# Kernel tuning notes

Measured on AMD Instinct MI355X. Metric: run time of the kernel, lower is better.

## Reference

```python
import jax, jax.numpy as jnp
import numpy as np

KH, KW = 3, 3  # kernel_size


def _extract_patches(x, kh, kw):
    # x: (B, Ci, H, W) -> patches: (B, Ci, kh*kw, H, W)
    # Matches torch.nn.functional.unfold channel-major, kernel row-major order.
    B, Ci, H, W = x.shape
    ph, pw = kh // 2, kw // 2
    xp = jnp.pad(x, ((0, 0), (0, 0), (ph, ph), (pw, pw)))
    shifts = [xp[:, :, i:i + H, j:j + W] for i in range(kh) for j in range(kw)]
    return jnp.stack(shifts, axis=2)  # (B, Ci, K, H, W)


def setup_inputs() -> dict:
    key = jax.random.key(0)
    k1, k2 = jax.random.split(key)
    B, Ci, Co, H, W = 2, 32, 32, 64, 64
    K = KH * KW
    input = jax.random.normal(k1, (B, Ci, H, W), dtype=jnp.float32)
    weights = jax.random.normal(k2, (B, Ci, K, Co, H, W), dtype=jnp.float32)
    return {"input": input, "weights": weights}


def reference(input, weights):
    # input:   (B, Ci, H, W)
    # weights: (B, Ci, K, Co, H, W) with K = KH*KW
    patches = _extract_patches(input, KH, KW)            # (B, Ci, K, H, W)
    # Per-pixel GEMV: out[b,o,h,w] = sum_{c,k} patches[b,c,k,h,w] * weights[b,c,k,o,h,w]
    out = jnp.einsum('bckhw,bckohw->bohw', patches, weights)
    return out
```

## Files before the change

kernel.cpp:

```cpp
#include <hip/hip_runtime.h>

constexpr int B  = 2;
constexpr int Ci = 32;
constexpr int K  = 9;
constexpr int Co = 32;
constexpr int H  = 64;
constexpr int W  = 64;

typedef float f32x4 __attribute__((ext_vector_type(4)));

__global__ __launch_bounds__(256) void glc2d_kernel(
    const float* __restrict__ input,
    const float* __restrict__ weights,
    float* __restrict__ out)
{
    __shared__ f32x4 partial[3][64];

    const int tid = threadIdx.x;
    const int q   = tid & 63;
    const int cq  = tid >> 6;
    const int g   = blockIdx.x * 64 + q;

    const int w4 = g & 15;
    const int h  = (g >> 4) & (H - 1);
    const int o  = (g >> 10) & (Co - 1);
    const int b  = g >> 15;
    const int w0 = w4 * 4;

    float acc0 = 0.f, acc1 = 0.f, acc2 = 0.f, acc3 = 0.f;

    const size_t plane = (size_t)H * W;
    const size_t cstride = (size_t)K * Co * plane;
    const size_t kstride = (size_t)Co * plane;

    const int c0 = cq * 8;
    const float* wp = weights + ((size_t)(b * Ci + c0) * K) * Co * plane
                              + (size_t)o * plane + (size_t)h * W + w0;
    const float* ip = input + ((size_t)b * Ci + c0) * plane + (size_t)h * W + w0;

    const bool has_left  = (w4 > 0);
    const bool has_right = (w4 < 15);

#pragma unroll 2
    for (int c = 0; c < 8; ++c) {
        const float* wcp = wp + (size_t)c * cstride;
        f32x4 wv[9];
#pragma unroll
        for (int k = 0; k < 9; ++k) {
            wv[k] = __builtin_nontemporal_load(
                reinterpret_cast<const f32x4*>(wcp + (size_t)k * kstride));
        }

        const float* icp = ip + (size_t)c * plane;
        float row[3][6];
#pragma unroll
        for (int r = 0; r < 3; ++r) {
            const int hh = h + r - 1;
            const bool hok = (hh >= 0) & (hh < H);
            f32x4 v;
            if (hok) {
                v = *reinterpret_cast<const f32x4*>(icp + (size_t)(r - 1) * W);
            } else {
                v = (f32x4)(0.f);
            }
            const float lf = __shfl_up(v.w, 1);
            const float rt = __shfl_down(v.x, 1);
            row[r][0] = has_left  ? lf : 0.f;
            row[r][1] = v.x;
            row[r][2] = v.y;
            row[r][3] = v.z;
            row[r][4] = v.w;
            row[r][5] = has_right ? rt : 0.f;
        }

#pragma unroll
        for (int k = 0; k < 9; ++k) {
            const int r = k / 3;
            const int qq = k % 3;
            acc0 = fmaf(row[r][qq + 0], wv[k].x, acc0);
            acc1 = fmaf(row[r][qq + 1], wv[k].y, acc1);
            acc2 = fmaf(row[r][qq + 2], wv[k].z, acc2);
            acc3 = fmaf(row[r][qq + 3], wv[k].w, acc3);
        }
    }

    f32x4 acc;
    acc.x = acc0; acc.y = acc1; acc.z = acc2; acc.w = acc3;
    if (cq) {
        partial[cq - 1][q] = acc;
    }
    __syncthreads();
    if (!cq) {
        const f32x4 p0 = partial[0][q];
        const f32x4 p1 = partial[1][q];
        const f32x4 p2 = partial[2][q];
        acc += p0 + p1 + p2;
        const size_t oidx = ((((size_t)b * Co + o) * H + h) * W + w0);
        *reinterpret_cast<f32x4*>(out + oidx) = acc;
    }
}

extern "C" void kernel_launch(void* const* d_in, const int* in_sizes, int n_in,
                              void* d_out, int out_size, void* d_ws, size_t ws_size,
                              hipStream_t stream)
{
    const float* input   = (const float*)d_in[0];
    const float* weights = (const float*)d_in[1];
    float* out = (float*)d_out;

    const int total_threads = B * Co * H * (W / 4) * 4;
    const int block = 256;
    const int grid = total_threads / block;
    glc2d_kernel<<<grid, block, 0, stream>>>(input, weights, out);
}
```

Before: 50.68 us.

## Split channel reduction across eight thread groups and stream weights per kernel row

The Ci reduction is now split 8 ways instead of 4: each 256-thread block handles 32 output slots, with eight groups of 4 channels each, and the grid doubles. Weight loads are issued per kernel row (3 vectors) rather than all 9 up front, which lowers register pressure, and launch bounds now request 8 blocks per CU. The aim is more waves in flight to hide memory latency on this bandwidth-bound weight stream. The cost is wider 32-lane shuffles within a wave, a larger final LDS reduction and fewer loads in flight per thread.

```diff
diff --git a/kernel.cpp b/kernel.cpp
--- a/kernel.cpp
+++ b/kernel.cpp
@@ -9,17 +9,17 @@
 
 typedef float f32x4 __attribute__((ext_vector_type(4)));
 
-__global__ __launch_bounds__(256) void glc2d_kernel(
+__global__ __launch_bounds__(256, 8) void glc2d_kernel(
     const float* __restrict__ input,
     const float* __restrict__ weights,
     float* __restrict__ out)
 {
-    __shared__ f32x4 partial[3][64];
+    __shared__ f32x4 partial[7][32];
 
-    const int tid = threadIdx.x;
-    const int q   = tid & 63;
-    const int cq  = tid >> 6;
-    const int g   = blockIdx.x * 64 + q;
+    const int tid  = threadIdx.x;
+    const int slot = tid & 31;
+    const int cq   = tid >> 5;
+    const int g    = blockIdx.x * 32 + slot;
 
     const int w4 = g & 15;
     const int h  = (g >> 4) & (H - 1);
@@ -33,7 +33,7 @@
     const size_t cstride = (size_t)K * Co * plane;
     const size_t kstride = (size_t)Co * plane;
 
-    const int c0 = cq * 8;
+    const int c0 = cq * 4;
     const float* wp = weights + ((size_t)(b * Ci + c0) * K) * Co * plane
                               + (size_t)o * plane + (size_t)h * W + w0;
     const float* ip = input + ((size_t)b * Ci + c0) * plane + (size_t)h * W + w0;
@@ -41,20 +41,19 @@
     const bool has_left  = (w4 > 0);
     const bool has_right = (w4 < 15);
 
-#pragma unroll 2
-    for (int c = 0; c < 8; ++c) {
+    for (int c = 0; c < 4; ++c) {
         const float* wcp = wp + (size_t)c * cstride;
-        f32x4 wv[9];
-#pragma unroll
-        for (int k = 0; k < 9; ++k) {
-            wv[k] = __builtin_nontemporal_load(
-                reinterpret_cast<const f32x4*>(wcp + (size_t)k * kstride));
-        }
+        const float* icp = ip + (size_t)c * plane;
 
-        const float* icp = ip + (size_t)c * plane;
-        float row[3][6];
 #pragma unroll
         for (int r = 0; r < 3; ++r) {
+            f32x4 wv0 = __builtin_nontemporal_load(
+                reinterpret_cast<const f32x4*>(wcp + (size_t)(3 * r + 0) * kstride));
+            f32x4 wv1 = __builtin_nontemporal_load(
+                reinterpret_cast<const f32x4*>(wcp + (size_t)(3 * r + 1) * kstride));
+            f32x4 wv2 = __builtin_nontemporal_load(
+                reinterpret_cast<const f32x4*>(wcp + (size_t)(3 * r + 2) * kstride));
+
             const int hh = h + r - 1;
             const bool hok = (hh >= 0) & (hh < H);
             f32x4 v;
@@ -65,36 +64,37 @@
             }
             const float lf = __shfl_up(v.w, 1);
             const float rt = __shfl_down(v.x, 1);
-            row[r][0] = has_left  ? lf : 0.f;
-            row[r][1] = v.x;
-            row[r][2] = v.y;
-            row[r][3] = v.z;
-            row[r][4] = v.w;
-            row[r][5] = has_right ? rt : 0.f;
-        }
+            const float e0 = has_left  ? lf : 0.f;
+            const float e5 = has_right ? rt : 0.f;
 
-#pragma unroll
-        for (int k = 0; k < 9; ++k) {
-            const int r = k / 3;
-            const int qq = k % 3;
-            acc0 = fmaf(row[r][qq + 0], wv[k].x, acc0);
-            acc1 = fmaf(row[r][qq + 1], wv[k].y, acc1);
-            acc2 = fmaf(row[r][qq + 2], wv[k].z, acc2);
-            acc3 = fmaf(row[r][qq + 3], wv[k].w, acc3);
+            acc0 = fmaf(e0,  wv0.x, acc0);
+            acc1 = fmaf(v.x, wv0.y, acc1);
+            acc2 = fmaf(v.y, wv0.z, acc2);
+            acc3 = fmaf(v.z, wv0.w, acc3);
+
+            acc0 = fmaf(v.x, wv1.x, acc0);
+            acc1 = fmaf(v.y, wv1.y, acc1);
+            acc2 = fmaf(v.z, wv1.z, acc2);
+            acc3 = fmaf(v.w, wv1.w, acc3);
+
+            acc0 = fmaf(v.y, wv2.x, acc0);
+            acc1 = fmaf(v.z, wv2.y, acc1);
+            acc2 = fmaf(v.w, wv2.z, acc2);
+            acc3 = fmaf(e5,  wv2.w, acc3);
         }
     }
 
     f32x4 acc;
     acc.x = acc0; acc.y = acc1; acc.z = acc2; acc.w = acc3;
     if (cq) {
-        partial[cq - 1][q] = acc;
+        partial[cq - 1][slot] = acc;
     }
     __syncthreads();
     if (!cq) {
-        const f32x4 p0 = partial[0][q];
-        const f32x4 p1 = partial[1][q];
-        const f32x4 p2 = partial[2][q];
-        acc += p0 + p1 + p2;
+#pragma unroll
+        for (int j = 0; j < 7; ++j) {
+            acc += partial[j][slot];
+        }
         const size_t oidx = ((((size_t)b * Co + o) * H + h) * W + w0);
         *reinterpret_cast<f32x4*>(out + oidx) = acc;
     }
@@ -108,7 +108,7 @@
     const float* weights = (const float*)d_in[1];
     float* out = (float*)d_out;
 
-    const int total_threads = B * Co * H * (W / 4) * 4;
+    const int total_threads = B * Co * H * (W / 4) * 8;
     const int block = 256;
     const int grid = total_threads / block;
     glc2d_kernel<<<grid, block, 0, stream>>>(input, weights, out);
```

New measurement: 183.6 us. 262% more time.
